# Kernel optimization log

Measured on AMD Instinct MI355X. Metric: run time of the kernel, lower is better.

Reference implementation:

```python
import jax, jax.numpy as jnp
import numpy as np

B, S, E, H = 512, 100, 256, 256
C_EXPLORE = 10.0  # tanh_exploration


def setup_inputs() -> dict:
    key = jax.random.key(0)
    ks = jax.random.split(key, 22)
    sH = 1.0 / np.sqrt(H)
    sE = 1.0 / np.sqrt(E)
    u = lambda k, shp, s: jax.random.uniform(k, shp, minval=-s, maxval=s, dtype=jnp.float32)
    return {
        "inputs": jax.random.uniform(ks[0], (B, 2, S), dtype=jnp.float32),  # 2D coords in [0,1)
        "emb": u(ks[1], (2, E), sE),
        "enc_Wih": u(ks[2], (4 * H, E), sH), "enc_Whh": u(ks[3], (4 * H, H), sH),
        "enc_bih": u(ks[4], (4 * H,), sH), "enc_bhh": u(ks[5], (4 * H,), sH),
        "dec_Wih": u(ks[6], (4 * H, E), sH), "dec_Whh": u(ks[7], (4 * H, H), sH),
        "dec_bih": u(ks[8], (4 * H,), sH), "dec_bhh": u(ks[9], (4 * H,), sH),
        "g_Wq": u(ks[10], (H, H), sH), "g_bq": u(ks[11], (H,), sH),
        "g_Wr": u(ks[12], (H, H), sH), "g_br": u(ks[13], (H,), sH),
        "g_V": u(ks[14], (H,), sH),
        "p_Wq": u(ks[15], (H, H), sH), "p_bq": u(ks[16], (H,), sH),
        "p_Wr": u(ks[17], (H, H), sH), "p_br": u(ks[18], (H,), sH),
        "p_V": u(ks[19], (H,), sH),
        "start": u(ks[20], (E,), sE),
    }


def _lstm_cell(x, h, c, Wih, Whh, bih, bhh):
    # torch LSTM gate order: input, forget, cell, output
    g = x @ Wih.T + h @ Whh.T + bih + bhh
    i, f, gg, o = jnp.split(g, 4, axis=-1)
    c = jax.nn.sigmoid(f) * c + jax.nn.sigmoid(i) * jnp.tanh(gg)
    return jax.nn.sigmoid(o) * jnp.tanh(c), c


def _forward(inputs, emb, enc_Wih, enc_Whh, enc_bih, enc_bhh,
             dec_Wih, dec_Whh, dec_bih, dec_bhh,
             g_Wq, g_bq, g_Wr, g_br, g_V,
             p_Wq, p_bq, p_Wr, p_br, p_V, start):
    # GraphEmbedding: per-position bmm([B,1,2],[B,2,E]) == single einsum
    embedded = jnp.einsum('bcs,ce->bse', inputs, emb)  # [B,S,E]

    h0 = jnp.zeros((B, H), jnp.float32)
    c0 = jnp.zeros((B, H), jnp.float32)

    def enc_step(carry, x_t):
        h, c = carry
        h, c = _lstm_cell(x_t, h, c, enc_Wih, enc_Whh, enc_bih, enc_bhh)
        return (h, c), h

    (h, c), outs = jax.lax.scan(enc_step, (h0, c0), embedded.transpose(1, 0, 2))
    enc = outs.transpose(1, 0, 2)  # encoder_outputs [B,S,H]

    # Conv1d(k=1) projection of encoder outputs is step-invariant: precompute once.
    ref_g = jnp.einsum('bsh,oh->bso', enc, g_Wr) + g_br  # [B,S,H]
    ref_p = jnp.einsum('bsh,oh->bso', enc, p_Wr) + p_br  # [B,S,H]

    keys = jax.random.split(jax.random.key(1), S)
    arange_b = jnp.arange(B)

    def attn(q, ref_proj, Wq, bq, V):
        qq = q @ Wq.T + bq  # [B,H]
        return jnp.einsum('h,bsh->bs', V, jnp.tanh(qq[:, None, :] + ref_proj))

    def step(carry, k):
        h, c, mask, idxs, valid, dec_in = carry
        h, c = _lstm_cell(dec_in, h, c, dec_Wih, dec_Whh, dec_bih, dec_bhh)
        # apply_mask_to_logits: mask grows by idxs only after first selection
        mask = jnp.where(valid, mask.at[arange_b, idxs].set(True), mask)
        # glimpse (n_glimpses = 1, use_tanh=False)
        lg = jnp.where(mask, -jnp.inf, attn(h, ref_g, g_Wq, g_bq, g_V))
        q = jnp.einsum('bsh,bs->bh', enc, jax.nn.softmax(lg, axis=-1))
        # pointer (use_tanh=True, C=10)
        lp = C_EXPLORE * jnp.tanh(attn(q, ref_p, p_Wq, p_bq, p_V))
        lp = jnp.where(mask, -jnp.inf, lp)
        probs = jax.nn.softmax(lp, axis=-1)
        idxs = jax.random.categorical(k, lp)  # multinomial(probs, 1)
        dec_in = embedded[arange_b, idxs]
        return (h, c, mask, idxs, jnp.array(True), dec_in), (probs, idxs)

    init = (h, c, jnp.zeros((B, S), bool), jnp.zeros((B,), jnp.int32),
            jnp.array(False), jnp.broadcast_to(start, (B, E)))
    _, (probs, idxs) = jax.lax.scan(step, init, keys)
    return probs, idxs  # [S,B,S] float, [S,B] int


def reference(inputs, emb, enc_Wih, enc_Whh, enc_bih, enc_bhh,
              dec_Wih, dec_Whh, dec_bih, dec_bhh,
              g_Wq, g_bq, g_Wr, g_br, g_V,
              p_Wq, p_bq, p_Wr, p_br, p_V, start):
    return _forward(inputs, emb, enc_Wih, enc_Whh, enc_bih, enc_bhh,
                    dec_Wih, dec_Whh, dec_bih, dec_bhh,
                    g_Wq, g_bq, g_Wr, g_br, g_V,
                    p_Wq, p_bq, p_Wr, p_br, p_V, start)
```

## Files before the change

### kernel.cpp

```cpp
#include <hip/hip_runtime.h>
#include <cstdint>
#include <math.h>

#define B_ 512
#define S_ 100
#define E_ 256
#define H_ 256

__device__ __forceinline__ float sigmoidf_(float x){ return 1.0f/(1.0f+expf(-x)); }

__device__ __forceinline__ void threefry2x32_(uint32_t k0, uint32_t k1,
                                              uint32_t c0, uint32_t c1,
                                              uint32_t& o0, uint32_t& o1){
  uint32_t ks2 = k0 ^ k1 ^ 0x1BD11BDAu;
  uint32_t x0 = c0 + k0, x1 = c1 + k1;
#define ROT_(x,d) (((x)<<(d))|((x)>>(32-(d))))
#define RND_(r) { x0 += x1; x1 = ROT_(x1,(r)); x1 ^= x0; }
  RND_(13) RND_(15) RND_(26) RND_(6)  x0 += k1;  x1 += ks2 + 1u;
  RND_(17) RND_(29) RND_(16) RND_(24) x0 += ks2; x1 += k0  + 2u;
  RND_(13) RND_(15) RND_(26) RND_(6)  x0 += k0;  x1 += k1  + 3u;
  RND_(17) RND_(29) RND_(16) RND_(24) x0 += k1;  x1 += ks2 + 4u;
  RND_(13) RND_(15) RND_(26) RND_(6)  x0 += ks2; x1 += k0  + 5u;
#undef RND_
#undef ROT_
  o0 = x0; o1 = x1;
}

__device__ __forceinline__ float gumbel_bits_(uint32_t bits){
  const float tiny = 1.175494350822287508e-38f;
  float u = __uint_as_float((bits >> 9) | 0x3f800000u) - 1.0f;
  u = fmaxf(tiny, u + tiny);
  return -logf(-logf(u));
}

__device__ __forceinline__ float wsum_(float v){
  #pragma unroll
  for (int d = 32; d > 0; d >>= 1) v += __shfl_xor(v, d, 64);
  return v;
}
__device__ __forceinline__ float wmax_(float v){
  #pragma unroll
  for (int d = 32; d > 0; d >>= 1) v = fmaxf(v, __shfl_xor(v, d, 64));
  return v;
}

struct KParams {
  const float *inputs, *emb;
  const float *gbq, *gV, *pbq, *pV;
  const float *gbr, *pbr;
  const float *start;
  const float *W4E, *W4D, *b4E, *b4D, *gWqT, *pWqT, *gWrT, *pWrT;
  float *enc, *refg, *refp;
  float *probs, *idxo;
};

struct PrepParams {
  const float *eWih, *eWhh, *ebih, *ebhh;
  const float *dWih, *dWhh, *dbih, *dbhh;
  const float *gWq, *pWq, *gWr, *pWr;
  float *W4E, *W4D, *b4E, *b4D, *gWqT, *pWqT, *gWrT, *pWrT;
};

__global__ __launch_bounds__(256) void prep_all(PrepParams P){
  const int i = blockIdx.x*256 + threadIdx.x;
  {
    const int g = i & 3, u = (i >> 2) & 255, k = i >> 10;
    const int row = g*256 + u;
    P.W4E[i] = (k < 256) ? P.eWih[row*256 + k] : P.eWhh[row*256 + (k-256)];
    P.W4D[i] = (k < 256) ? P.dWih[row*256 + k] : P.dWhh[row*256 + (k-256)];
  }
  if (i < 65536) {
    const int r = i >> 8, cc = i & 255;
    P.gWqT[i] = P.gWq[cc*256 + r];
    P.pWqT[i] = P.pWq[cc*256 + r];
    P.gWrT[i] = P.gWr[cc*256 + r];
    P.pWrT[i] = P.pWr[cc*256 + r];
  }
  if (i < 1024) {
    const int g = i & 3, u = i >> 2;
    P.b4E[i] = P.ebih[g*256 + u] + P.ebhh[g*256 + u];
    P.b4D[i] = P.dbih[g*256 + u] + P.dbhh[g*256 + u];
  }
}

__global__ __launch_bounds__(256, 1) void pointer_net_perb(KParams P)
{
  const int tid  = threadIdx.x;
  const int u    = tid;
  const int lane = tid & 63;
  const int wv   = tid >> 6;
  const int b0   = blockIdx.x * 2;

  __shared__ float embL[512];
  __shared__ float xs[512];
  __shared__ float hs[512];
  __shared__ float es[20*256];
  __shared__ float qqL[512];
  __shared__ float qL[512];
  __shared__ float pqL[512];
  __shared__ float lgL[128];
  __shared__ float alphaL[256];
  __shared__ float lpL[128];
  __shared__ int   maskL[256];
  __shared__ int   selL[2];

  embL[tid]       = P.emb[tid];
  embL[256 + tid] = P.emb[256 + tid];
  maskL[tid] = 0;
  if (tid < 2) selL[tid] = -1;
  hs[tid*2] = 0.f; hs[tid*2 + 1] = 0.f;
  float c0 = 0.f, c1 = 0.f;
  __syncthreads();

  for (int t = 0; t < S_; ++t) {
    for (int i = tid; i < 512; i += 256) {
      const int k = i >> 1, r = i & 1, b = b0 + r;
      xs[i] = P.inputs[b*200 + t]*embL[k] + P.inputs[b*200 + 100 + t]*embL[256 + k];
    }
    __syncthreads();

    float a0x=0.f,a0y=0.f,a0z=0.f,a0w=0.f, a1x=0.f,a1y=0.f,a1z=0.f,a1w=0.f;
    const float* wp = P.W4E + (size_t)u*4;
    #pragma unroll 8
    for (int k = 0; k < 256; ++k) {
      const float4 w = *(const float4*)(wp + (size_t)k*1024);
      const float2 x = *(const float2*)(xs + k*2);
      a0x += x.x*w.x; a0y += x.x*w.y; a0z += x.x*w.z; a0w += x.x*w.w;
      a1x += x.y*w.x; a1y += x.y*w.y; a1z += x.y*w.z; a1w += x.y*w.w;
    }
    #pragma unroll 8
    for (int k = 256; k < 512; ++k) {
      const float4 w = *(const float4*)(wp + (size_t)k*1024);
      const float2 x = *(const float2*)(hs + (k - 256)*2);
      a0x += x.x*w.x; a0y += x.x*w.y; a0z += x.x*w.z; a0w += x.x*w.w;
      a1x += x.y*w.x; a1y += x.y*w.y; a1z += x.y*w.z; a1w += x.y*w.w;
    }
    __syncthreads();

    const float4 bb4 = *(const float4*)(P.b4E + u*4);
    {
      const float gi = a0x + bb4.x, gf = a0y + bb4.y, gg = a0z + bb4.z, go = a0w + bb4.w;
      const float cN = sigmoidf_(gf)*c0 + sigmoidf_(gi)*tanhf(gg);
      const float hN = sigmoidf_(go)*tanhf(cN);
      c0 = cN; hs[u*2] = hN;
      P.enc[((size_t)b0*S_ + t)*H_ + u] = hN;
    }
    {
      const float gi = a1x + bb4.x, gf = a1y + bb4.y, gg = a1z + bb4.z, go = a1w + bb4.w;
      const float cN = sigmoidf_(gf)*c1 + sigmoidf_(gi)*tanhf(gg);
      const float hN = sigmoidf_(go)*tanhf(cN);
      c1 = cN; hs[u*2 + 1] = hN;
      P.enc[((size_t)(b0+1)*S_ + t)*H_ + u] = hN;
    }
    __syncthreads();
  }

  for (int bb = 0; bb < 2; ++bb) {
    const int b = b0 + bb;
    for (int s0 = 0; s0 < S_; s0 += 20) {
      for (int i = tid; i < 20*256; i += 256)
        es[i] = P.enc[((size_t)b*S_ + s0 + (i >> 8))*H_ + (i & 255)];
      __syncthreads();
      float accg[20], accp[20];
      #pragma unroll
      for (int s = 0; s < 20; ++s) { accg[s] = 0.f; accp[s] = 0.f; }
      #pragma unroll 4
      for (int k = 0; k < 256; ++k) {
        const float wg = P.gWrT[k*256 + u];
        const float wpv = P.pWrT[k*256 + u];
        #pragma unroll
        for (int s = 0; s < 20; ++s) {
          const float xk = es[s*256 + k];
          accg[s] += xk*wg; accp[s] += xk*wpv;
        }
      }
      const float bg = P.gbr[u], bp = P.pbr[u];
      #pragma unroll
      for (int s = 0; s < 20; ++s) {
        P.refg[((size_t)b*S_ + s0 + s)*H_ + u] = accg[s] + bg;
        P.refp[((size_t)b*S_ + s0 + s)*H_ + u] = accp[s] + bp;
      }
      __syncthreads();
    }
  }

  for (int t = 0; t < S_; ++t) {
    for (int i = tid; i < 512; i += 256) {
      const int k = i >> 1, r = i & 1, b = b0 + r;
      const int s = selL[r];
      float v;
      if (s < 0) v = P.start[k];
      else       v = P.inputs[b*200 + s]*embL[k] + P.inputs[b*200 + 100 + s]*embL[256 + k];
      xs[i] = v;
    }
    __syncthreads();

    float a0x=0.f,a0y=0.f,a0z=0.f,a0w=0.f, a1x=0.f,a1y=0.f,a1z=0.f,a1w=0.f;
    const float* wp = P.W4D + (size_t)u*4;
    #pragma unroll 8
    for (int k = 0; k < 256; ++k) {
      const float4 w = *(const float4*)(wp + (size_t)k*1024);
      const float2 x = *(const float2*)(xs + k*2);
      a0x += x.x*w.x; a0y += x.x*w.y; a0z += x.x*w.z; a0w += x.x*w.w;
      a1x += x.y*w.x; a1y += x.y*w.y; a1z += x.y*w.z; a1w += x.y*w.w;
    }
    #pragma unroll 8
    for (int k = 256; k < 512; ++k) {
      const float4 w = *(const float4*)(wp + (size_t)k*1024);
      const float2 x = *(const float2*)(hs + (k - 256)*2);
      a0x += x.x*w.x; a0y += x.x*w.y; a0z += x.x*w.z; a0w += x.x*w.w;
      a1x += x.y*w.x; a1y += x.y*w.y; a1z += x.y*w.z; a1w += x.y*w.w;
    }
    __syncthreads();

    const float4 bb4 = *(const float4*)(P.b4D + u*4);
    {
      const float gi = a0x + bb4.x, gf = a0y + bb4.y, gg = a0z + bb4.z, go = a0w + bb4.w;
      const float cN = sigmoidf_(gf)*c0 + sigmoidf_(gi)*tanhf(gg);
      const float hN = sigmoidf_(go)*tanhf(cN);
      c0 = cN; hs[u*2] = hN;
    }
    {
      const float gi = a1x + bb4.x, gf = a1y + bb4.y, gg = a1z + bb4.z, go = a1w + bb4.w;
      const float cN = sigmoidf_(gf)*c1 + sigmoidf_(gi)*tanhf(gg);
      const float hN = sigmoidf_(go)*tanhf(cN);
      c1 = cN; hs[u*2 + 1] = hN;
    }
    __syncthreads();

    {
      float a0 = P.gbq[tid], a1 = a0;
      #pragma unroll 4
      for (int k = 0; k < 256; ++k) {
        const float w = P.gWqT[k*256 + tid];
        a0 += hs[k*2]*w; a1 += hs[k*2 + 1]*w;
      }
      qqL[tid] = a0; qqL[256 + tid] = a1;
    }
    __syncthreads();

    for (int bb = 0; bb < 2; ++bb) {
      const float* rg = P.refg + (size_t)(b0+bb)*S_*H_;
      const int* mk = maskL + bb*128;
      for (int is = 0; is < 25; ++is) {
        const int s = is*4 + wv;
        float pp = 0.f;
        #pragma unroll
        for (int j = 0; j < 4; ++j) {
          const int hh = lane + 64*j;
          pp += P.gV[hh] * tanhf(qqL[bb*256 + hh] + rg[s*256 + hh]);
        }
        pp = wsum_(pp);
        if (lane == 0) lgL[s] = mk[s] ? -INFINITY : pp;
      }
      __syncthreads();
      if (wv == 0) {
        const float v0 = lgL[lane];
        const float v1 = (lane + 64 < S_) ? lgL[lane + 64] : -INFINITY;
        const float m  = wmax_(fmaxf(v0, v1));
        const float e0 = expf(v0 - m);
        const float e1 = (lane + 64 < S_) ? expf(v1 - m) : 0.f;
        const float smm = wsum_(e0 + e1);
        alphaL[bb*128 + lane] = e0 / smm;
        if (lane + 64 < S_) alphaL[bb*128 + lane + 64] = e1 / smm;
      }
      __syncthreads();
    }

    {
      const float* e0p = P.enc + (size_t)b0*S_*H_;
      const float* e1p = P.enc + (size_t)(b0+1)*S_*H_;
      float a0 = 0.f, a1 = 0.f;
      for (int s = 0; s < S_; ++s) {
        a0 += alphaL[s]       * e0p[s*256 + tid];
        a1 += alphaL[128 + s] * e1p[s*256 + tid];
      }
      qL[tid] = a0; qL[256 + tid] = a1;
    }
    __syncthreads();

    {
      float a0 = P.pbq[tid], a1 = a0;
      #pragma unroll 4
      for (int k = 0; k < 256; ++k) {
        const float w = P.pWqT[k*256 + tid];
        a0 += qL[k]*w; a1 += qL[256 + k]*w;
      }
      pqL[tid] = a0; pqL[256 + tid] = a1;
    }
    __syncthreads();

    for (int bb = 0; bb < 2; ++bb) {
      const int b = b0 + bb;
      const float* rp = P.refp + (size_t)b*S_*H_;
      const int* mk = maskL + bb*128;
      for (int is = 0; is < 25; ++is) {
        const int s = is*4 + wv;
        float pp = 0.f;
        #pragma unroll
        for (int j = 0; j < 4; ++j) {
          const int hh = lane + 64*j;
          pp += P.pV[hh] * tanhf(pqL[bb*256 + hh] + rp[s*256 + hh]);
        }
        pp = wsum_(pp);
        if (lane == 0) {
          const float v = 10.0f * tanhf(pp);
          lpL[s] = mk[s] ? -INFINITY : v;
        }
      }
      __syncthreads();
      if (wv == 0) {
        const float v0 = lpL[lane];
        const float v1 = (lane + 64 < S_) ? lpL[lane + 64] : -INFINITY;
        const float m  = wmax_(fmaxf(v0, v1));
        const float e0 = expf(v0 - m);
        const float e1 = (lane + 64 < S_) ? expf(v1 - m) : 0.f;
        const float smm = wsum_(e0 + e1);
        float* po = P.probs + ((size_t)t*B_ + b)*S_;
        po[lane] = e0 / smm;
        if (lane + 64 < S_) po[lane + 64] = e1 / smm;

        uint32_t k0, k1; threefry2x32_(0u, 1u, 0u, (uint32_t)t, k0, k1);
        uint32_t r0, r1;
        threefry2x32_(k0, k1, 0u, (uint32_t)(b*S_ + lane), r0, r1);
        float z0 = v0 + gumbel_bits_(r0 ^ r1);
        float z1 = -INFINITY;
        if (lane + 64 < S_) {
          uint32_t q0, q1;
          threefry2x32_(k0, k1, 0u, (uint32_t)(b*S_ + lane + 64), q0, q1);
          z1 = v1 + gumbel_bits_(q0 ^ q1);
        }
        float bv; int bi;
        if (z1 > z0) { bv = z1; bi = lane + 64; } else { bv = z0; bi = lane; }
        #pragma unroll
        for (int d = 32; d > 0; d >>= 1) {
          const float ov = __shfl_xor(bv, d, 64);
          const int   oi = __shfl_xor(bi, d, 64);
          if (ov > bv || (ov == bv && oi < bi)) { bv = ov; bi = oi; }
        }
        if (lane == 0) {
          P.idxo[t*B_ + b] = (float)bi;
          selL[bb] = bi;
          maskL[bb*128 + bi] = 1;
        }
      }
      __syncthreads();
    }
  }
}

extern "C" void kernel_launch(void* const* d_in, const int* in_sizes, int n_in,
                              void* d_out, int out_size, void* d_ws, size_t ws_size,
                              hipStream_t stream) {
  (void)in_sizes; (void)n_in; (void)out_size; (void)ws_size;

  float* ws = (float*)d_ws;
  size_t o = 0;
  float* W4E  = ws + o; o += (size_t)512*1024;
  float* W4D  = ws + o; o += (size_t)512*1024;
  float* b4E  = ws + o; o += 1024;
  float* b4D  = ws + o; o += 1024;
  float* gWqT = ws + o; o += 65536;
  float* pWqT = ws + o; o += 65536;
  float* gWrT = ws + o; o += 65536;
  float* pWrT = ws + o; o += 65536;
  float* enc  = ws + o; o += (size_t)B_*S_*H_;
  float* refg = ws + o; o += (size_t)B_*S_*H_;
  float* refp = ws + o; o += (size_t)B_*S_*H_;

  PrepParams PP;
  PP.eWih = (const float*)d_in[2];  PP.eWhh = (const float*)d_in[3];
  PP.ebih = (const float*)d_in[4];  PP.ebhh = (const float*)d_in[5];
  PP.dWih = (const float*)d_in[6];  PP.dWhh = (const float*)d_in[7];
  PP.dbih = (const float*)d_in[8];  PP.dbhh = (const float*)d_in[9];
  PP.gWq  = (const float*)d_in[10]; PP.pWq  = (const float*)d_in[15];
  PP.gWr  = (const float*)d_in[12]; PP.pWr  = (const float*)d_in[17];
  PP.W4E = W4E; PP.W4D = W4D; PP.b4E = b4E; PP.b4D = b4D;
  PP.gWqT = gWqT; PP.pWqT = pWqT; PP.gWrT = gWrT; PP.pWrT = pWrT;

  KParams P;
  P.inputs = (const float*)d_in[0];
  P.emb    = (const float*)d_in[1];
  P.gbq    = (const float*)d_in[11];
  P.gbr    = (const float*)d_in[13];
  P.gV     = (const float*)d_in[14];
  P.pbq    = (const float*)d_in[16];
  P.pbr    = (const float*)d_in[18];
  P.pV     = (const float*)d_in[19];
  P.start  = (const float*)d_in[20];
  P.W4E = W4E; P.W4D = W4D; P.b4E = b4E; P.b4D = b4D;
  P.gWqT = gWqT; P.pWqT = pWqT; P.gWrT = gWrT; P.pWrT = pWrT;
  P.enc = enc; P.refg = refg; P.refp = refp;
  P.probs = (float*)d_out;
  P.idxo  = P.probs + (size_t)S_*B_*S_;

  prep_all<<<2048, 256, 0, stream>>>(PP);
  pointer_net_perb<<<256, 256, 0, stream>>>(P);
}
```

Before: 23.28 ms.

## Double threads per block, splitting gate and batch work across halves

Launches the fused pointer-network kernel with 512 threads instead of 256. Each half of the block handles one of the two batch rows for the LSTM gates, the reference projections and the query projections, and gate partial sums are exchanged through shared memory. The two attention passes now run for both batch rows at once, using wave groups, instead of looping over them. Reference projections are stored in a swizzled layout so attention can use float4 loads, and the query weights are repacked for float4 reads. This adds parallelism to a latency-bound recurrent loop, at the cost of an extra shared-memory exchange and higher register and shared-memory pressure per block.

New measurement: 26.00 ms. 1.12x slower.

```diff
diff --git a/kernel.cpp b/kernel.cpp
--- a/kernel.cpp
+++ b/kernel.cpp
@@ -49,8 +49,8 @@
   const float *gbq, *gV, *pbq, *pV;
   const float *gbr, *pbr;
   const float *start;
-  const float *W4E, *W4D, *b4E, *b4D, *gWqT, *pWqT, *gWrT, *pWrT;
-  float *enc, *refg, *refp;
+  const float *W4E, *W4D, *b4E, *b4D, *gWqS, *pWqS, *gWrT, *pWrT;
+  float *enc, *rgS, *rpS;
   float *probs, *idxo;
 };
 
@@ -58,294 +58,287 @@
   const float *eWih, *eWhh, *ebih, *ebhh;
   const float *dWih, *dWhh, *dbih, *dbhh;
   const float *gWq, *pWq, *gWr, *pWr;
-  float *W4E, *W4D, *b4E, *b4D, *gWqT, *pWqT, *gWrT, *pWrT;
+  float *W4E, *W4D, *b4E, *b4D, *gWqS, *pWqS, *gWrT, *pWrT;
 };
 
 __global__ __launch_bounds__(256) void prep_all(PrepParams P){
   const int i = blockIdx.x*256 + threadIdx.x;
   {
-    const int g = i & 3, u = (i >> 2) & 255, k = i >> 10;
-    const int row = g*256 + u;
+    const int g = i & 3, u2 = (i >> 2) & 255, k = i >> 10;
+    const int row = g*256 + u2;
     P.W4E[i] = (k < 256) ? P.eWih[row*256 + k] : P.eWhh[row*256 + (k-256)];
     P.W4D[i] = (k < 256) ? P.dWih[row*256 + k] : P.dWhh[row*256 + (k-256)];
   }
   if (i < 65536) {
     const int r = i >> 8, cc = i & 255;
-    P.gWqT[i] = P.gWq[cc*256 + r];
-    P.pWqT[i] = P.pWq[cc*256 + r];
     P.gWrT[i] = P.gWr[cc*256 + r];
     P.pWrT[i] = P.pWr[cc*256 + r];
+    const int j = i & 3, uq = (i >> 2) & 255, kq = i >> 10;
+    P.gWqS[i] = P.gWq[uq*256 + kq*4 + j];
+    P.pWqS[i] = P.pWq[uq*256 + kq*4 + j];
   }
   if (i < 1024) {
-    const int g = i & 3, u = i >> 2;
-    P.b4E[i] = P.ebih[g*256 + u] + P.ebhh[g*256 + u];
-    P.b4D[i] = P.dbih[g*256 + u] + P.dbhh[g*256 + u];
-  }
-}
-
-__global__ __launch_bounds__(256, 1) void pointer_net_perb(KParams P)
+    const int g = i & 3, u2 = i >> 2;
+    P.b4E[i] = P.ebih[g*256 + u2] + P.ebhh[g*256 + u2];
+    P.b4D[i] = P.dbih[g*256 + u2] + P.dbhh[g*256 + u2];
+  }
+}
+
+__global__ __launch_bounds__(512, 2) void pointer_net_perb(KParams P)
 {
   const int tid  = threadIdx.x;
-  const int u    = tid;
+  const int u    = tid & 255;
+  const int half = tid >> 8;
   const int lane = tid & 63;
   const int wv   = tid >> 6;
+  const int wvL  = wv & 3;
+  const int wbb  = wv >> 2;
   const int b0   = blockIdx.x * 2;
 
   __shared__ float embL[512];
   __shared__ float xs[512];
   __shared__ float hs[512];
-  __shared__ float es[20*256];
-  __shared__ float qqL[512];
-  __shared__ float qL[512];
-  __shared__ float pqL[512];
-  __shared__ float lgL[128];
-  __shared__ float alphaL[256];
-  __shared__ float lpL[128];
   __shared__ int   maskL[256];
   __shared__ int   selL[2];
-
-  embL[tid]       = P.emb[tid];
-  embL[256 + tid] = P.emb[256 + tid];
-  maskL[tid] = 0;
+  __shared__ union UU {
+    float es[2][5120];
+    struct {
+      float gbuf[2048];
+      float qqL[512], qL[512], pqL[512];
+      float lg[256], alpha[256], lp[256];
+    } s;
+  } uu;
+
+  embL[tid] = P.emb[tid];
+  if (tid < 256) maskL[tid] = 0;
   if (tid < 2) selL[tid] = -1;
-  hs[tid*2] = 0.f; hs[tid*2 + 1] = 0.f;
-  float c0 = 0.f, c1 = 0.f;
+  hs[tid] = 0.f;
+  float cc = 0.f;
+  const float gvx = P.gV[lane], gvy = P.gV[lane+64], gvz = P.gV[lane+128], gvw = P.gV[lane+192];
+  const float pvx = P.pV[lane], pvy = P.pV[lane+64], pvz = P.pV[lane+128], pvw = P.pV[lane+192];
   __syncthreads();
 
   for (int t = 0; t < S_; ++t) {
-    for (int i = tid; i < 512; i += 256) {
-      const int k = i >> 1, r = i & 1, b = b0 + r;
-      xs[i] = P.inputs[b*200 + t]*embL[k] + P.inputs[b*200 + 100 + t]*embL[256 + k];
-    }
-    __syncthreads();
-
-    float a0x=0.f,a0y=0.f,a0z=0.f,a0w=0.f, a1x=0.f,a1y=0.f,a1z=0.f,a1w=0.f;
-    const float* wp = P.W4E + (size_t)u*4;
+    { const int k = tid >> 1, r = tid & 1, b = b0 + r;
+      xs[tid] = P.inputs[b*200 + t]*embL[k] + P.inputs[b*200 + 100 + t]*embL[256 + k]; }
+    __syncthreads();
+
+    float a0x=0.f,a0y=0.f,a1x=0.f,a1y=0.f;
+    const float* wp = P.W4E + (size_t)u*4 + half*2;
     #pragma unroll 8
     for (int k = 0; k < 256; ++k) {
-      const float4 w = *(const float4*)(wp + (size_t)k*1024);
+      const float2 w = *(const float2*)(wp + (size_t)k*1024);
       const float2 x = *(const float2*)(xs + k*2);
-      a0x += x.x*w.x; a0y += x.x*w.y; a0z += x.x*w.z; a0w += x.x*w.w;
-      a1x += x.y*w.x; a1y += x.y*w.y; a1z += x.y*w.z; a1w += x.y*w.w;
+      a0x += x.x*w.x; a0y += x.x*w.y; a1x += x.y*w.x; a1y += x.y*w.y;
     }
     #pragma unroll 8
     for (int k = 256; k < 512; ++k) {
-      const float4 w = *(const float4*)(wp + (size_t)k*1024);
-      const float2 x = *(const float2*)(hs + (k - 256)*2);
-      a0x += x.x*w.x; a0y += x.x*w.y; a0z += x.x*w.z; a0w += x.x*w.w;
-      a1x += x.y*w.x; a1y += x.y*w.y; a1z += x.y*w.z; a1w += x.y*w.w;
-    }
-    __syncthreads();
-
-    const float4 bb4 = *(const float4*)(P.b4E + u*4);
+      const float2 w = *(const float2*)(wp + (size_t)k*1024);
+      const float2 x = *(const float2*)(hs + (k-256)*2);
+      a0x += x.x*w.x; a0y += x.x*w.y; a1x += x.y*w.x; a1y += x.y*w.y;
+    }
+    uu.s.gbuf[u*8 + 0 + half*2]     = a0x;
+    uu.s.gbuf[u*8 + 0 + half*2 + 1] = a0y;
+    uu.s.gbuf[u*8 + 4 + half*2]     = a1x;
+    uu.s.gbuf[u*8 + 4 + half*2 + 1] = a1y;
+    __syncthreads();
     {
-      const float gi = a0x + bb4.x, gf = a0y + bb4.y, gg = a0z + bb4.z, go = a0w + bb4.w;
-      const float cN = sigmoidf_(gf)*c0 + sigmoidf_(gi)*tanhf(gg);
+      const float4 g4  = *(const float4*)(uu.s.gbuf + u*8 + half*4);
+      const float4 bb4 = *(const float4*)(P.b4E + u*4);
+      const float gi = g4.x + bb4.x, gf = g4.y + bb4.y, gg = g4.z + bb4.z, go = g4.w + bb4.w;
+      const float cN = sigmoidf_(gf)*cc + sigmoidf_(gi)*tanhf(gg);
       const float hN = sigmoidf_(go)*tanhf(cN);
-      c0 = cN; hs[u*2] = hN;
-      P.enc[((size_t)b0*S_ + t)*H_ + u] = hN;
-    }
-    {
-      const float gi = a1x + bb4.x, gf = a1y + bb4.y, gg = a1z + bb4.z, go = a1w + bb4.w;
-      const float cN = sigmoidf_(gf)*c1 + sigmoidf_(gi)*tanhf(gg);
-      const float hN = sigmoidf_(go)*tanhf(cN);
-      c1 = cN; hs[u*2 + 1] = hN;
-      P.enc[((size_t)(b0+1)*S_ + t)*H_ + u] = hN;
-    }
-    __syncthreads();
-  }
-
-  for (int bb = 0; bb < 2; ++bb) {
-    const int b = b0 + bb;
-    for (int s0 = 0; s0 < S_; s0 += 20) {
-      for (int i = tid; i < 20*256; i += 256)
-        es[i] = P.enc[((size_t)b*S_ + s0 + (i >> 8))*H_ + (i & 255)];
-      __syncthreads();
-      float accg[20], accp[20];
-      #pragma unroll
-      for (int s = 0; s < 20; ++s) { accg[s] = 0.f; accp[s] = 0.f; }
-      #pragma unroll 4
-      for (int k = 0; k < 256; ++k) {
-        const float wg = P.gWrT[k*256 + u];
-        const float wpv = P.pWrT[k*256 + u];
-        #pragma unroll
-        for (int s = 0; s < 20; ++s) {
-          const float xk = es[s*256 + k];
-          accg[s] += xk*wg; accp[s] += xk*wpv;
-        }
-      }
-      const float bg = P.gbr[u], bp = P.pbr[u];
+      cc = cN; hs[u*2 + half] = hN;
+      P.enc[((size_t)(b0+half)*S_ + t)*H_ + u] = hN;
+    }
+    __syncthreads();
+  }
+
+  for (int s0 = 0; s0 < S_; s0 += 20) {
+    for (int i = u; i < 5120; i += 256)
+      uu.es[half][i] = P.enc[((size_t)(b0+half)*S_ + s0 + (i >> 8))*H_ + (i & 255)];
+    __syncthreads();
+    float accg[20], accp[20];
+    #pragma unroll
+    for (int s = 0; s < 20; ++s) { accg[s] = 0.f; accp[s] = 0.f; }
+    #pragma unroll 4
+    for (int k = 0; k < 256; ++k) {
+      const float wg  = P.gWrT[k*256 + u];
+      const float wpv = P.pWrT[k*256 + u];
       #pragma unroll
       for (int s = 0; s < 20; ++s) {
-        P.refg[((size_t)b*S_ + s0 + s)*H_ + u] = accg[s] + bg;
-        P.refp[((size_t)b*S_ + s0 + s)*H_ + u] = accp[s] + bp;
-      }
-      __syncthreads();
-    }
+        const float xk = uu.es[half][s*256 + k];
+        accg[s] += xk*wg; accp[s] += xk*wpv;
+      }
+    }
+    const float bg = P.gbr[u], bp = P.pbr[u];
+    const int usw = (u & 63)*4 + (u >> 6);
+    #pragma unroll
+    for (int s = 0; s < 20; ++s) {
+      P.rgS[((size_t)(b0+half)*S_ + s0 + s)*256 + usw] = accg[s] + bg;
+      P.rpS[((size_t)(b0+half)*S_ + s0 + s)*256 + usw] = accp[s] + bp;
+    }
+    __syncthreads();
   }
 
   for (int t = 0; t < S_; ++t) {
-    for (int i = tid; i < 512; i += 256) {
-      const int k = i >> 1, r = i & 1, b = b0 + r;
+    { const int k = tid >> 1, r = tid & 1, b = b0 + r;
       const int s = selL[r];
-      float v;
-      if (s < 0) v = P.start[k];
-      else       v = P.inputs[b*200 + s]*embL[k] + P.inputs[b*200 + 100 + s]*embL[256 + k];
-      xs[i] = v;
-    }
-    __syncthreads();
-
-    float a0x=0.f,a0y=0.f,a0z=0.f,a0w=0.f, a1x=0.f,a1y=0.f,a1z=0.f,a1w=0.f;
-    const float* wp = P.W4D + (size_t)u*4;
+      xs[tid] = (s < 0) ? P.start[k]
+              : P.inputs[b*200 + s]*embL[k] + P.inputs[b*200 + 100 + s]*embL[256 + k]; }
+    __syncthreads();
+
+    float a0x=0.f,a0y=0.f,a1x=0.f,a1y=0.f;
+    const float* wp = P.W4D + (size_t)u*4 + half*2;
     #pragma unroll 8
     for (int k = 0; k < 256; ++k) {
-      const float4 w = *(const float4*)(wp + (size_t)k*1024);
+      const float2 w = *(const float2*)(wp + (size_t)k*1024);
       const float2 x = *(const float2*)(xs + k*2);
-      a0x += x.x*w.x; a0y += x.x*w.y; a0z += x.x*w.z; a0w += x.x*w.w;
-      a1x += x.y*w.x; a1y += x.y*w.y; a1z += x.y*w.z; a1w += x.y*w.w;
+      a0x += x.x*w.x; a0y += x.x*w.y; a1x += x.y*w.x; a1y += x.y*w.y;
     }
     #pragma unroll 8
     for (int k = 256; k < 512; ++k) {
-      const float4 w = *(const float4*)(wp + (size_t)k*1024);
-      const float2 x = *(const float2*)(hs + (k - 256)*2);
-      a0x += x.x*w.x; a0y += x.x*w.y; a0z += x.x*w.z; a0w += x.x*w.w;
-      a1x += x.y*w.x; a1y += x.y*w.y; a1z += x.y*w.z; a1w += x.y*w.w;
-    }
-    __syncthreads();
-
-    const float4 bb4 = *(const float4*)(P.b4D + u*4);
+      const float2 w = *(const float2*)(wp + (size_t)k*1024);
+      const float2 x = *(const float2*)(hs + (k-256)*2);
+      a0x += x.x*w.x; a0y += x.x*w.y; a1x += x.y*w.x; a1y += x.y*w.y;
+    }
+    uu.s.gbuf[u*8 + 0 + half*2]     = a0x;
+    uu.s.gbuf[u*8 + 0 + half*2 + 1] = a0y;
+    uu.s.gbuf[u*8 + 4 + half*2]     = a1x;
+    uu.s.gbuf[u*8 + 4 + half*2 + 1] = a1y;
+    __syncthreads();
     {
-      const float gi = a0x + bb4.x, gf = a0y + bb4.y, gg = a0z + bb4.z, go = a0w + bb4.w;
-      const float cN = sigmoidf_(gf)*c0 + sigmoidf_(gi)*tanhf(gg);
+      const float4 g4  = *(const float4*)(uu.s.gbuf + u*8 + half*4);
+      const float4 bb4 = *(const float4*)(P.b4D + u*4);
+      const float gi = g4.x + bb4.x, gf = g4.y + bb4.y, gg = g4.z + bb4.z, go = g4.w + bb4.w;
+      const float cN = sigmoidf_(gf)*cc + sigmoidf_(gi)*tanhf(gg);
       const float hN = sigmoidf_(go)*tanhf(cN);
-      c0 = cN; hs[u*2] = hN;
-    }
+      cc = cN; hs[u*2 + half] = hN;
+    }
+    __syncthreads();
+
+    { float a = P.gbq[u];
+      const float4* wq = (const float4*)P.gWqS + u;
+      #pragma unroll 4
+      for (int kq = 0; kq < 64; ++kq) {
+        const float4 w = wq[(size_t)kq*256];
+        a += hs[(4*kq+0)*2 + half]*w.x;
+        a += hs[(4*kq+1)*2 + half]*w.y;
+        a += hs[(4*kq+2)*2 + half]*w.z;
+        a += hs[(4*kq+3)*2 + half]*w.w;
+      }
+      uu.s.qqL[half*256 + u] = a; }
+    __syncthreads();
+
     {
-      const float gi = a1x + bb4.x, gf = a1y + bb4.y, gg = a1z + bb4.z, go = a1w + bb4.w;
-      const float cN = sigmoidf_(gf)*c1 + sigmoidf_(gi)*tanhf(gg);
-      const float hN = sigmoidf_(go)*tanhf(cN);
-      c1 = cN; hs[u*2 + 1] = hN;
-    }
+      const float q0 = uu.s.qqL[wbb*256 + lane];
+      const float q1 = uu.s.qqL[wbb*256 + lane + 64];
+      const float q2 = uu.s.qqL[wbb*256 + lane + 128];
+      const float q3 = uu.s.qqL[wbb*256 + lane + 192];
+      const float* rgb = P.rgS + (size_t)(b0+wbb)*S_*H_;
+      const int* mk = maskL + wbb*128;
+      for (int is = 0; is < 25; ++is) {
+        const int s = is*4 + wvL;
+        const float4 r4 = *(const float4*)(rgb + s*256 + lane*4);
+        float pp = gvx*tanhf(q0 + r4.x);
+        pp += gvy*tanhf(q1 + r4.y);
+        pp += gvz*tanhf(q2 + r4.z);
+        pp += gvw*tanhf(q3 + r4.w);
+        pp = wsum_(pp);
+        if (lane == 0) uu.s.lg[wbb*128 + s] = mk[s] ? -INFINITY : pp;
+      }
+    }
+    __syncthreads();
+    if (wvL == 0) {
+      const float v0 = uu.s.lg[wbb*128 + lane];
+      const float v1 = (lane + 64 < S_) ? uu.s.lg[wbb*128 + lane + 64] : -INFINITY;
+      const float m  = wmax_(fmaxf(v0, v1));
+      const float e0 = expf(v0 - m);
+      const float e1 = (lane + 64 < S_) ? expf(v1 - m) : 0.f;
+      const float sm = wsum_(e0 + e1);
+      uu.s.alpha[wbb*128 + lane] = e0 / sm;
+      if (lane + 64 < S_) uu.s.alpha[wbb*128 + lane + 64] = e1 / sm;
+    }
+    __syncthreads();
+
+    { const float* eb = P.enc + (size_t)(b0+half)*S_*H_;
+      float a = 0.f;
+      for (int s = 0; s < S_; ++s) a += uu.s.alpha[half*128 + s] * eb[s*256 + u];
+      uu.s.qL[half*256 + u] = a; }
+    __syncthreads();
+
+    { float a = P.pbq[u];
+      const float4* wq = (const float4*)P.pWqS + u;
+      #pragma unroll 4
+      for (int kq = 0; kq < 64; ++kq) {
+        const float4 w = wq[(size_t)kq*256];
+        a += uu.s.qL[half*256 + 4*kq+0]*w.x;
+        a += uu.s.qL[half*256 + 4*kq+1]*w.y;
+        a += uu.s.qL[half*256 + 4*kq+2]*w.z;
+        a += uu.s.qL[half*256 + 4*kq+3]*w.w;
+      }
+      uu.s.pqL[half*256 + u] = a; }
     __syncthreads();
 
     {
-      float a0 = P.gbq[tid], a1 = a0;
-      #pragma unroll 4
-      for (int k = 0; k < 256; ++k) {
-        const float w = P.gWqT[k*256 + tid];
-        a0 += hs[k*2]*w; a1 += hs[k*2 + 1]*w;
-      }
-      qqL[tid] = a0; qqL[256 + tid] = a1;
-    }
-    __syncthreads();
-
-    for (int bb = 0; bb < 2; ++bb) {
-      const float* rg = P.refg + (size_t)(b0+bb)*S_*H_;
-      const int* mk = maskL + bb*128;
+      const float q0 = uu.s.pqL[wbb*256 + lane];
+      const float q1 = uu.s.pqL[wbb*256 + lane + 64];
+      const float q2 = uu.s.pqL[wbb*256 + lane + 128];
+      const float q3 = uu.s.pqL[wbb*256 + lane + 192];
+      const float* rpb = P.rpS + (size_t)(b0+wbb)*S_*H_;
+      const int* mk = maskL + wbb*128;
       for (int is = 0; is < 25; ++is) {
-        const int s = is*4 + wv;
-        float pp = 0.f;
-        #pragma unroll
-        for (int j = 0; j < 4; ++j) {
-          const int hh = lane + 64*j;
-          pp += P.gV[hh] * tanhf(qqL[bb*256 + hh] + rg[s*256 + hh]);
-        }
-        pp = wsum_(pp);
-        if (lane == 0) lgL[s] = mk[s] ? -INFINITY : pp;
-      }
-      __syncthreads();
-      if (wv == 0) {
-        const float v0 = lgL[lane];
-        const float v1 = (lane + 64 < S_) ? lgL[lane + 64] : -INFINITY;
-        const float m  = wmax_(fmaxf(v0, v1));
-        const float e0 = expf(v0 - m);
-        const float e1 = (lane + 64 < S_) ? expf(v1 - m) : 0.f;
-        const float smm = wsum_(e0 + e1);
-        alphaL[bb*128 + lane] = e0 / smm;
-        if (lane + 64 < S_) alphaL[bb*128 + lane + 64] = e1 / smm;
-      }
-      __syncthreads();
-    }
-
-    {
-      const float* e0p = P.enc + (size_t)b0*S_*H_;
-      const float* e1p = P.enc + (size_t)(b0+1)*S_*H_;
-      float a0 = 0.f, a1 = 0.f;
-      for (int s = 0; s < S_; ++s) {
-        a0 += alphaL[s]       * e0p[s*256 + tid];
-        a1 += alphaL[128 + s] * e1p[s*256 + tid];
-      }
-      qL[tid] = a0; qL[256 + tid] = a1;
-    }
-    __syncthreads();
-
-    {
-      float a0 = P.pbq[tid], a1 = a0;
-      #pragma unroll 4
-      for (int k = 0; k < 256; ++k) {
-        const float w = P.pWqT[k*256 + tid];
-        a0 += qL[k]*w; a1 += qL[256 + k]*w;
-      }
-      pqL[tid] = a0; pqL[256 + tid] = a1;
-    }
-    __syncthreads();
-
-    for (int bb = 0; bb < 2; ++bb) {
-      const int b = b0 + bb;
-      const float* rp = P.refp + (size_t)b*S_*H_;
-      const int* mk = maskL + bb*128;
-      for (int is = 0; is < 25; ++is) {
-        const int s = is*4 + wv;
-        float pp = 0.f;
-        #pragma unroll
-        for (int j = 0; j < 4; ++j) {
-          const int hh = lane + 64*j;
-          pp += P.pV[hh] * tanhf(pqL[bb*256 + hh] + rp[s*256 + hh]);
-        }
+        const int s = is*4 + wvL;
+        const float4 r4 = *(const float4*)(rpb + s*256 + lane*4);
+        float pp = pvx*tanhf(q0 + r4.x);
+        pp += pvy*tanhf(q1 + r4.y);
+        pp += pvz*tanhf(q2 + r4.z);
+        pp += pvw*tanhf(q3 + r4.w);
         pp = wsum_(pp);
         if (lane == 0) {
           const float v = 10.0f * tanhf(pp);
-          lpL[s] = mk[s] ? -INFINITY : v;
+          uu.s.lp[wbb*128 + s] = mk[s] ? -INFINITY : v;
         }
       }
-      __syncthreads();
-      if (wv == 0) {
-        const float v0 = lpL[lane];
-        const float v1 = (lane + 64 < S_) ? lpL[lane + 64] : -INFINITY;
-        const float m  = wmax_(fmaxf(v0, v1));
-        const float e0 = expf(v0 - m);
-        const float e1 = (lane + 64 < S_) ? expf(v1 - m) : 0.f;
-        const float smm = wsum_(e0 + e1);
-        float* po = P.probs + ((size_t)t*B_ + b)*S_;
-        po[lane] = e0 / smm;
-        if (lane + 64 < S_) po[lane + 64] = e1 / smm;
-
-        uint32_t k0, k1; threefry2x32_(0u, 1u, 0u, (uint32_t)t, k0, k1);
-        uint32_t r0, r1;
-        threefry2x32_(k0, k1, 0u, (uint32_t)(b*S_ + lane), r0, r1);
-        float z0 = v0 + gumbel_bits_(r0 ^ r1);
-        float z1 = -INFINITY;
-        if (lane + 64 < S_) {
-          uint32_t q0, q1;
-          threefry2x32_(k0, k1, 0u, (uint32_t)(b*S_ + lane + 64), q0, q1);
-          z1 = v1 + gumbel_bits_(q0 ^ q1);
-        }
-        float bv; int bi;
-        if (z1 > z0) { bv = z1; bi = lane + 64; } else { bv = z0; bi = lane; }
-        #pragma unroll
-        for (int d = 32; d > 0; d >>= 1) {
-          const float ov = __shfl_xor(bv, d, 64);
-          const int   oi = __shfl_xor(bi, d, 64);
-          if (ov > bv || (ov == bv && oi < bi)) { bv = ov; bi = oi; }
-        }
-        if (lane == 0) {
-          P.idxo[t*B_ + b] = (float)bi;
-          selL[bb] = bi;
-          maskL[bb*128 + bi] = 1;
-        }
-      }
-      __syncthreads();
-    }
+    }
+    __syncthreads();
+    if (wvL == 0) {
+      const int b = b0 + wbb;
+      const float v0 = uu.s.lp[wbb*128 + lane];
+      const float v1 = (lane + 64 < S_) ? uu.s.lp[wbb*128 + lane + 64] : -INFINITY;
+      const float m  = wmax_(fmaxf(v0, v1));
+      const float e0 = expf(v0 - m);
+      const float e1 = (lane + 64 < S_) ? expf(v1 - m) : 0.f;
+      const float sm = wsum_(e0 + e1);
+      float* po = P.probs + ((size_t)t*B_ + b)*S_;
+      po[lane] = e0 / sm;
+      if (lane + 64 < S_) po[lane + 64] = e1 / sm;
+
+      uint32_t k0, k1; threefry2x32_(0u, 1u, 0u, (uint32_t)t, k0, k1);
+      uint32_t r0, r1;
+      threefry2x32_(k0, k1, 0u, (uint32_t)(b*S_ + lane), r0, r1);
+      float z0 = v0 + gumbel_bits_(r0 ^ r1);
+      float z1 = -INFINITY;
+      if (lane + 64 < S_) {
+        uint32_t q0b, q1b;
+        threefry2x32_(k0, k1, 0u, (uint32_t)(b*S_ + lane + 64), q0b, q1b);
+        z1 = v1 + gumbel_bits_(q0b ^ q1b);
+      }
+      float bv; int bi;
+      if (z1 > z0) { bv = z1; bi = lane + 64; } else { bv = z0; bi = lane; }
+      #pragma unroll
+      for (int d = 32; d > 0; d >>= 1) {
+        const float ov = __shfl_xor(bv, d, 64);
+        const int   oi = __shfl_xor(bi, d, 64);
+        if (ov > bv || (ov == bv && oi < bi)) { bv = ov; bi = oi; }
+      }
+      if (lane == 0) {
+        P.idxo[t*B_ + b] = (float)bi;
+        selL[wbb] = bi;
+        maskL[wbb*128 + bi] = 1;
+      }
+    }
+    __syncthreads();
   }
 }
 
@@ -360,13 +353,13 @@
   float* W4D  = ws + o; o += (size_t)512*1024;
   float* b4E  = ws + o; o += 1024;
   float* b4D  = ws + o; o += 1024;
-  float* gWqT = ws + o; o += 65536;
-  float* pWqT = ws + o; o += 65536;
+  float* gWqS = ws + o; o += 65536;
+  float* pWqS = ws + o; o += 65536;
   float* gWrT = ws + o; o += 65536;
   float* pWrT = ws + o; o += 65536;
   float* enc  = ws + o; o += (size_t)B_*S_*H_;
-  float* refg = ws + o; o += (size_t)B_*S_*H_;
-  float* refp = ws + o; o += (size_t)B_*S_*H_;
+  float* rgS  = ws + o; o += (size_t)B_*S_*H_;
+  float* rpS  = ws + o; o += (size_t)B_*S_*H_;
 
   PrepParams PP;
   PP.eWih = (const float*)d_in[2];  PP.eWhh = (const float*)d_in[3];
@@ -376,7 +369,7 @@
   PP.gWq  = (const float*)d_in[10]; PP.pWq  = (const float*)d_in[15];
   PP.gWr  = (const float*)d_in[12]; PP.pWr  = (const float*)d_in[17];
   PP.W4E = W4E; PP.W4D = W4D; PP.b4E = b4E; PP.b4D = b4D;
-  PP.gWqT = gWqT; PP.pWqT = pWqT; PP.gWrT = gWrT; PP.pWrT = pWrT;
+  PP.gWqS = gWqS; PP.pWqS = pWqS; PP.gWrT = gWrT; PP.pWrT = pWrT;
 
   KParams P;
   P.inputs = (const float*)d_in[0];
@@ -389,11 +382,11 @@
   P.pV     = (const float*)d_in[19];
   P.start  = (const float*)d_in[20];
   P.W4E = W4E; P.W4D = W4D; P.b4E = b4E; P.b4D = b4D;
-  P.gWqT = gWqT; P.pWqT = pWqT; P.gWrT = gWrT; P.pWrT = pWrT;
-  P.enc = enc; P.refg = refg; P.refp = refp;
+  P.gWqS = gWqS; P.pWqS = pWqS; P.gWrT = gWrT; P.pWrT = pWrT;
+  P.enc = enc; P.rgS = rgS; P.rpS = rpS;
   P.probs = (float*)d_out;
   P.idxo  = P.probs + (size_t)S_*B_*S_;
 
   prep_all<<<2048, 256, 0, stream>>>(PP);
-  pointer_net_perb<<<256, 256, 0, stream>>>(P);
-}
+  pointer_net_perb<<<256, 512, 0, stream>>>(P);
+}
```
